# Kernel tuning notes

Measured on AMD Instinct MI355X. Metric: run time of the kernel, lower is better.

The kernel has to match this reference:

```python
import jax, jax.numpy as jnp
import numpy as np

LN_EPS = 1e-5
GATE_EPS = 1e-9
TOP_K = 2
CAP_FACTOR = 1.0


def reference(x, gamma, beta, wg, W1, b1, W2, b2):
    B, S, H = x.shape
    E = wg.shape[1]
    T = B * S
    K = TOP_K
    C = int(np.ceil(K * T / E * CAP_FACTOR))  # per-expert capacity

    xf = x.reshape(T, H)
    # LayerNorm
    mu = jnp.mean(xf, axis=-1, keepdims=True)
    var = jnp.mean(jnp.square(xf - mu), axis=-1, keepdims=True)
    xn = (xf - mu) * jax.lax.rsqrt(var + LN_EPS) * gamma + beta

    # Gating (DeepSpeed top-k gate, softmax over experts)
    logits = xn @ wg                       # [T,E]
    gates = jax.nn.softmax(logits, axis=-1)
    vals, idx = jax.lax.top_k(gates, K)    # [T,K]

    # Capacity-aware positions: slot j priorities come after slots <j counts
    counts = jnp.zeros((E,), jnp.int32)
    pos_l, keep_l = [], []
    for j in range(K):
        oh = jax.nn.one_hot(idx[:, j], E, dtype=jnp.int32)  # [T,E]
        loc = jnp.cumsum(oh, axis=0) - 1 + counts[None, :]
        pos = jnp.sum(loc * oh, axis=1)                      # [T]
        counts = counts + jnp.sum(oh, axis=0)
        pos_l.append(pos)
        keep_l.append(pos < C)
    pos_k = jnp.stack(pos_l, axis=1)                         # [T,K]
    keep_k = jnp.stack(keep_l, axis=1)                       # [T,K]

    # Normalize kept gate values (DeepSpeed normalizes after capacity drop)
    kept = vals * keep_k.astype(vals.dtype)
    w = kept / (jnp.sum(kept, axis=1, keepdims=True) + GATE_EPS)  # [T,K]

    # Load-balancing aux loss (top-1 assignment counts, DeepSpeed style)
    me = jnp.mean(gates, axis=0)
    ce = jnp.mean(jax.nn.one_hot(idx[:, 0], E, dtype=gates.dtype), axis=0)
    l_aux = jnp.mean(me * ce) * E * E

    # Dispatch: scatter tokens into [E, C+1, H]; dropped tokens go to slot C (discarded)
    buf = jnp.zeros((E, C + 1, H), xn.dtype)
    pos_pad = jnp.where(keep_k, pos_k, C)                    # [T,K]
    for j in range(K):
        buf = buf.at[idx[:, j], pos_pad[:, j]].add(xn)

    # Grouped expert MLP
    h1 = jax.nn.gelu(jnp.einsum('ech,ehf->ecf', buf, W1) + b1[:, None, :], approximate=False)
    y = jnp.einsum('ecf,efh->ech', h1, W2) + b2[:, None, :]   # [E,C+1,H]

    # Combine: gather each token's expert outputs, weight, sum
    outf = jnp.zeros((T, H), x.dtype)
    for j in range(K):
        outf = outf + w[:, j, None] * y[idx[:, j], pos_pad[:, j]]

    out = x + outf.reshape(B, S, H)
    return out, l_aux, counts.astype(jnp.float32)


def setup_inputs() -> dict:
    key = jax.random.key(0)
    ks = jax.random.split(key, 6)
    H, E, F = 1024, 8, 4096
    x = jax.random.normal(ks[0], (2, 2048, H), jnp.float32)
    return {
        'x': x,
        'gamma': jnp.ones((H,), jnp.float32),
        'beta': jnp.zeros((H,), jnp.float32),
        'wg': jax.random.normal(ks[1], (H, E), jnp.float32) * 0.02,
        'W1': jax.random.normal(ks[2], (E, H, F), jnp.float32) * 0.02,
        'b1': jnp.zeros((E, F), jnp.float32),
        'W2': jax.random.normal(ks[3], (E, F, H), jnp.float32) * 0.02,
        'b2': jnp.zeros((E, H), jnp.float32),
    }
```

## Files before the change

kernel.cpp:

```cpp
#include <hip/hip_runtime.h>
#include <hip/hip_bf16.h>
#include <math.h>


#define T_TOK 4096
#define HD 1024
#define NE 8
#define FD 4096
#define CAPN 1024

typedef __attribute__((ext_vector_type(8))) short short8;
typedef __attribute__((ext_vector_type(4))) float f32x4;

__device__ __forceinline__ unsigned short f2b(float f) {
  __hip_bfloat16 h = __float2bfloat16(f);
  unsigned short u;
  __builtin_memcpy(&u, &h, 2);
  return u;
}

__global__ __launch_bounds__(256) void k_ln_gate(
    const float* __restrict__ x, const float* __restrict__ gamma,
    const float* __restrict__ beta, const float* __restrict__ wg,
    unsigned short* __restrict__ xn, float* __restrict__ gates,
    float2* __restrict__ vals, int2* __restrict__ eidx) {
  const int t = blockIdx.x;
  const int tid = threadIdx.x;
  const int lane = tid & 63, wid = tid >> 6;
  __shared__ float red[4];
  __shared__ float pr[4][8];

  const float4 v = ((const float4*)(x + (size_t)t * HD))[tid];
  float s = v.x + v.y + v.z + v.w;
#pragma unroll
  for (int o = 32; o > 0; o >>= 1) s += __shfl_down(s, o);
  if (lane == 0) red[wid] = s;
  __syncthreads();
  const float mean = (red[0] + red[1] + red[2] + red[3]) * (1.0f / HD);
  float dv[4];
  dv[0] = v.x - mean; dv[1] = v.y - mean; dv[2] = v.z - mean; dv[3] = v.w - mean;
  float q = dv[0]*dv[0] + dv[1]*dv[1] + dv[2]*dv[2] + dv[3]*dv[3];
  __syncthreads();
#pragma unroll
  for (int o = 32; o > 0; o >>= 1) q += __shfl_down(q, o);
  if (lane == 0) red[wid] = q;
  __syncthreads();
  const float var = (red[0] + red[1] + red[2] + red[3]) * (1.0f / HD);
  const float rs = 1.0f / sqrtf(var + 1e-5f);

  const float4 gm = ((const float4*)gamma)[tid];
  const float4 bt = ((const float4*)beta)[tid];
  float xv[4];
  xv[0] = dv[0] * rs * gm.x + bt.x;
  xv[1] = dv[1] * rs * gm.y + bt.y;
  xv[2] = dv[2] * rs * gm.z + bt.z;
  xv[3] = dv[3] * rs * gm.w + bt.w;
  ushort4 o4;
  o4.x = f2b(xv[0]); o4.y = f2b(xv[1]); o4.z = f2b(xv[2]); o4.w = f2b(xv[3]);
  ((ushort4*)(xn + (size_t)t * HD))[tid] = o4;

  float p[8];
#pragma unroll
  for (int e = 0; e < 8; e++) p[e] = 0.f;
  const int c0 = tid * 4;
#pragma unroll
  for (int i = 0; i < 4; i++) {
    const float4 w0 = ((const float4*)(wg + (size_t)(c0 + i) * NE))[0];
    const float4 w1 = ((const float4*)(wg + (size_t)(c0 + i) * NE))[1];
    p[0] += xv[i] * w0.x; p[1] += xv[i] * w0.y;
    p[2] += xv[i] * w0.z; p[3] += xv[i] * w0.w;
    p[4] += xv[i] * w1.x; p[5] += xv[i] * w1.y;
    p[6] += xv[i] * w1.z; p[7] += xv[i] * w1.w;
  }
#pragma unroll
  for (int e = 0; e < 8; e++)
#pragma unroll
    for (int o = 32; o > 0; o >>= 1) p[e] += __shfl_down(p[e], o);
  if (lane == 0) {
#pragma unroll
    for (int e = 0; e < 8; e++) pr[wid][e] = p[e];
  }
  __syncthreads();
  if (tid == 0) {
    float lg[8];
#pragma unroll
    for (int e = 0; e < 8; e++) lg[e] = pr[0][e] + pr[1][e] + pr[2][e] + pr[3][e];
    float mx = lg[0];
#pragma unroll
    for (int e = 1; e < 8; e++) mx = fmaxf(mx, lg[e]);
    float ex[8], sum = 0.f;
#pragma unroll
    for (int e = 0; e < 8; e++) { ex[e] = expf(lg[e] - mx); sum += ex[e]; }
    const float inv = 1.0f / sum;
    float g[8];
#pragma unroll
    for (int e = 0; e < 8; e++) { g[e] = ex[e] * inv; gates[(size_t)t * 8 + e] = g[e]; }
    int i0 = 0;
    for (int e = 1; e < 8; e++) if (g[e] > g[i0]) i0 = e;
    int i1 = (i0 == 0) ? 1 : 0;
    for (int e = 0; e < 8; e++) if (e != i0 && g[e] > g[i1]) i1 = e;
    vals[t] = make_float2(g[i0], g[i1]);
    eidx[t] = make_int2(i0, i1);
  }
}

__global__ __launch_bounds__(256) void k_scan(
    const int2* __restrict__ eidx, const float* __restrict__ gates,
    int* __restrict__ ppad, float* __restrict__ out_tail) {
  __shared__ int s0[T_TOK], s1[T_TOK];
  __shared__ float mw[3][8];
  __shared__ int ce_sh[8], cnt_sh[8];
  const int tid = threadIdx.x;
  const int lane = tid & 63, wid = tid >> 6;
  for (int i = tid; i < T_TOK; i += 256) {
    int2 e2 = eidx[i];
    s0[i] = e2.x; s1[i] = e2.y;
  }
  __syncthreads();
  if (wid == 0) {
    const unsigned long long lt = (lane == 63) ? 0x7fffffffffffffffull
                                               : ((1ull << lane) - 1ull);
    int cnt[8];
#pragma unroll
    for (int e = 0; e < 8; e++) cnt[e] = 0;
    for (int j = 0; j < 2; j++) {
      const int* sj = j ? s1 : s0;
      for (int base = 0; base < T_TOK; base += 64) {
        const int my = sj[base + lane];
        int pos = 0;
#pragma unroll
        for (int e = 0; e < 8; e++) {
          unsigned long long m = __ballot(my == e);
          if (my == e) pos = cnt[e] + __popcll(m & lt);
          cnt[e] += __popcll(m);
        }
        ppad[(base + lane) * 2 + j] = (pos < CAPN) ? pos : CAPN;
      }
      if (j == 0 && lane == 0) {
#pragma unroll
        for (int e = 0; e < 8; e++) ce_sh[e] = cnt[e];
      }
    }
    if (lane == 0) {
#pragma unroll
      for (int e = 0; e < 8; e++) cnt_sh[e] = cnt[e];
    }
  } else {
    float acc[8];
#pragma unroll
    for (int e = 0; e < 8; e++) acc[e] = 0.f;
    for (int t = tid - 64; t < T_TOK; t += 192) {
      const float4 a = ((const float4*)(gates + (size_t)t * 8))[0];
      const float4 b = ((const float4*)(gates + (size_t)t * 8))[1];
      acc[0] += a.x; acc[1] += a.y; acc[2] += a.z; acc[3] += a.w;
      acc[4] += b.x; acc[5] += b.y; acc[6] += b.z; acc[7] += b.w;
    }
#pragma unroll
    for (int e = 0; e < 8; e++)
#pragma unroll
      for (int o = 32; o > 0; o >>= 1) acc[e] += __shfl_down(acc[e], o);
    if (lane == 0) {
#pragma unroll
      for (int e = 0; e < 8; e++) mw[wid - 1][e] = acc[e];
    }
  }
  __syncthreads();
  if (tid == 0) {
    float la = 0.f;
#pragma unroll
    for (int e = 0; e < 8; e++) {
      const float me = (mw[0][e] + mw[1][e] + mw[2][e]) * (1.0f / T_TOK);
      la += me * ((float)ce_sh[e] * (1.0f / T_TOK));
    }
    out_tail[0] = la * 8.0f;
#pragma unroll
    for (int e = 0; e < 8; e++) out_tail[1 + e] = (float)cnt_sh[e];
  }
}

__global__ __launch_bounds__(128) void k_scatter(
    const unsigned short* __restrict__ xn, const int2* __restrict__ eidx,
    const int* __restrict__ ppad, unsigned short* __restrict__ buf) {
  const int b = blockIdx.x;
  const int t = b >> 1, j = b & 1;
  const int pp = ppad[2 * t + j];
  if (pp >= CAPN) return;
  const int2 e2 = eidx[t];
  const int e = j ? e2.y : e2.x;
  const uint4* s = (const uint4*)(xn + (size_t)t * HD);
  uint4* d = (uint4*)(buf + ((size_t)e * CAPN + pp) * HD);
  d[threadIdx.x] = s[threadIdx.x];
}

__global__ __launch_bounds__(256) void k_convT(
    const float* __restrict__ Win, unsigned short* __restrict__ Wout,
    int R, int C) {
  __shared__ __align__(16) unsigned short tile[64][72];
  const int e = blockIdx.z;
  const int c0 = blockIdx.x * 64, r0 = blockIdx.y * 64;
  const int tid = threadIdx.x;
  const int r = tid >> 2, qq = tid & 3;
  const float* src = Win + ((size_t)e * R + r0 + r) * C + c0;
#pragma unroll
  for (int i = 0; i < 4; i++) {
    const int cc = qq * 16 + i * 4;
    const float4 v = *(const float4*)(src + cc);
    tile[cc + 0][r] = f2b(v.x);
    tile[cc + 1][r] = f2b(v.y);
    tile[cc + 2][r] = f2b(v.z);
    tile[cc + 3][r] = f2b(v.w);
  }
  __syncthreads();
  const int cr = tid >> 2;
  unsigned short* dst = Wout + ((size_t)e * C + c0 + cr) * R + r0 + qq * 16;
  *(uint4*)(dst + 0) = *(const uint4*)&tile[cr][qq * 16];
  *(uint4*)(dst + 8) = *(const uint4*)&tile[cr][qq * 16 + 8];
}

#define GLL16(SRC, DSTOFF) __builtin_amdgcn_global_load_lds( \
    (const __attribute__((address_space(1))) void*)(SRC), \
    (__attribute__((address_space(3))) void*)(smem + (DSTOFF)), 16, 0, 0)

#define STAGE_A(T) { const size_t ko = (size_t)(T) * 32; const int rbo = ((T)&3)*32768; \
  GLL16(gA + ko + oA0, rbo + ldsAd); \
  GLL16(gA + ko + oA1, rbo + 8192 + ldsAd); }

#define STAGE_B(T) { const size_t ko = (size_t)(T) * 32; const int rbo = ((T)&3)*32768; \
  GLL16(gB + ko + oA0, rbo + ldsBd); \
  GLL16(gB + ko + oA1, rbo + 8192 + ldsBd); }

#define TILE(T, DOST, VMW) { \
  const unsigned char* rb = smem + ((T)&3)*32768; \
  short8 af[4], bfv[4]; \
  _Pragma("unroll") for (int i = 0; i < 4; ++i) { \
    af[i]  = *(const short8*)(rb + offA + i*1024); \
    bfv[i] = *(const short8*)(rb + offB + i*1024); } \
  if (DOST) { STAGE_A((T)+3); } \
  asm volatile("s_barrier" ::: "memory"); \
  __builtin_amdgcn_s_setprio(1); \
  _Pragma("unroll") for (int mi = 0; mi < 4; ++mi) \
    _Pragma("unroll") for (int ni = 0; ni < 4; ++ni) \
      acc[mi][ni] = __builtin_amdgcn_mfma_f32_16x16x32_bf16(af[mi], bfv[ni], acc[mi][ni], 0, 0, 0); \
  __builtin_amdgcn_s_setprio(0); \
  _Pragma("unroll") for (int i = 0; i < 4; ++i) \
    af[i] = *(const short8*)(rb + offA + 4096 + i*1024); \
  if (DOST) { STAGE_B((T)+3); } \
  asm volatile("s_waitcnt lgkmcnt(0)" ::: "memory"); \
  asm volatile("s_waitcnt vmcnt(" #VMW ")" ::: "memory"); \
  asm volatile("s_barrier" ::: "memory"); \
  __builtin_amdgcn_s_setprio(1); \
  _Pragma("unroll") for (int mi = 0; mi < 4; ++mi) \
    _Pragma("unroll") for (int ni = 0; ni < 4; ++ni) \
      acc[4+mi][ni] = __builtin_amdgcn_mfma_f32_16x16x32_bf16(af[mi], bfv[ni], acc[4+mi][ni], 0, 0, 0); \
  __builtin_amdgcn_s_setprio(0); \
}

template <int MODE, int SPLITK>
__global__ __launch_bounds__(512, 2) void k_gemm256(
    const unsigned short* __restrict__ A, const unsigned short* __restrict__ Bt,
    const float* __restrict__ bias, void* __restrict__ out) {
  constexpr int K = MODE ? FD : HD;
  constexpr int N = MODE ? HD : FD;
  constexpr int KLOC = K / SPLITK;
  constexpr int NT = KLOC / 32;
  constexpr int NBT = N / 256;

  __shared__ __align__(16) unsigned char smem[4 * 32768];

  const int tid = threadIdx.x;
  const int lane = tid & 63, wid = tid >> 6;
  const int l15 = lane & 15, lq = lane >> 4;
  const int wr = wid >> 2, wc = wid & 3;

  const int nwg = gridDim.x;
  const int per = nwg >> 3;
  const int lin = blockIdx.x;
  const int swz = (lin & 7) * per + (lin >> 3);
  const int mt = swz & 31;
  const int rest = swz >> 5;
  const int nt = rest % NBT;
  const int z = rest / NBT;

  const int e = mt >> 2;
  const size_t m0 = (size_t)mt * 256;
  const int n0 = nt * 256;
  const unsigned short* gA = A + m0 * (size_t)K + (size_t)z * KLOC;
  const unsigned short* gB = Bt + ((size_t)e * N + n0) * (size_t)K + (size_t)z * KLOC;

  const int LA0 = tid * 16, LA1 = 8192 + tid * 16;
  const int r0s = LA0 >> 6, c0s = (LA0 >> 4) & 3;
  const int r1s = LA1 >> 6, c1s = (LA1 >> 4) & 3;
  const size_t oA0 = (size_t)r0s * K + (size_t)(c0s ^ ((r0s >> 1) & 3)) * 8;
  const size_t oA1 = (size_t)r1s * K + (size_t)(c1s ^ ((r1s >> 1) & 3)) * 8;
  const int ldsAd = wid * 1024;
  const int ldsBd = 16384 + wid * 1024;

  const int rA = wr * 128 + l15;
  const int offA = rA * 64 + ((lq ^ ((rA >> 1) & 3)) << 4);
  const int rB = wc * 64 + l15;
  const int offB = 16384 + rB * 64 + ((lq ^ ((rB >> 1) & 3)) << 4);

  f32x4 acc[8][4];
  const f32x4 fz = {0.f, 0.f, 0.f, 0.f};
#pragma unroll
  for (int mi = 0; mi < 8; mi++)
#pragma unroll
    for (int ni = 0; ni < 4; ni++) acc[mi][ni] = fz;

  STAGE_A(0); STAGE_B(0);
  STAGE_A(1); STAGE_B(1);
  STAGE_A(2); STAGE_B(2);
  asm volatile("s_waitcnt vmcnt(8)" ::: "memory");
  asm volatile("s_barrier" ::: "memory");

  for (int t = 0; t <= NT - 4; ++t) { TILE(t, true, 8); }
  TILE(NT - 3, false, 4);
  TILE(NT - 2, false, 0);
  TILE(NT - 1, false, 63);

  if (MODE == 0) {
    unsigned short* o = (unsigned short*)out;
    const float* brow = bias + (size_t)e * N;
#pragma unroll
    for (int mi = 0; mi < 8; ++mi)
#pragma unroll
      for (int ni = 0; ni < 4; ++ni) {
        const int col = n0 + wc * 64 + ni * 16 + l15;
        const float bv = brow[col];
#pragma unroll
        for (int r = 0; r < 4; ++r) {
          const size_t row = m0 + wr * 128 + mi * 16 + lq * 4 + r;
          const float pre = acc[mi][ni][r] + bv;
          const float g = 0.5f * pre * (1.0f + erff(pre * 0.70710678118654752f));
          o[row * (size_t)N + col] = f2b(g);
        }
      }
  } else {
    float* yp = (float*)out + (size_t)z * (8192ull * 1024ull);
#pragma unroll
    for (int mi = 0; mi < 8; ++mi)
#pragma unroll
      for (int ni = 0; ni < 4; ++ni) {
        const int col = n0 + wc * 64 + ni * 16 + l15;
#pragma unroll
        for (int r = 0; r < 4; ++r) {
          const size_t row = m0 + wr * 128 + mi * 16 + lq * 4 + r;
          yp[row * (size_t)N + col] = acc[mi][ni][r];
        }
      }
  }
}
#undef TILE
#undef STAGE_A
#undef STAGE_B
#undef GLL16

template <int SPLIT>
__global__ __launch_bounds__(256) void k_combine(
    const float* __restrict__ x, const float* __restrict__ y0,
    const float* __restrict__ y1, const float* __restrict__ b2,
    const int2* __restrict__ eidx, const int* __restrict__ ppad,
    const float2* __restrict__ vals, float* __restrict__ out) {
  const int t = blockIdx.x, tid = threadIdx.x;
  const float2 v = vals[t];
  const int2 e2 = eidx[t];
  const int p0 = ppad[2 * t], p1 = ppad[2 * t + 1];
  const float k0 = (p0 < CAPN) ? v.x : 0.f;
  const float k1 = (p1 < CAPN) ? v.y : 0.f;
  const float inv = 1.0f / (k0 + k1 + 1e-9f);
  const float w0 = k0 * inv, w1 = k1 * inv;
  float4 o = ((const float4*)(x + (size_t)t * HD))[tid];
  if (p0 < CAPN) {
    const size_t s = ((size_t)e2.x * CAPN + p0) * HD;
    float4 a = ((const float4*)(y0 + s))[tid];
    if (SPLIT == 2) {
      const float4 b = ((const float4*)(y1 + s))[tid];
      a.x += b.x; a.y += b.y; a.z += b.z; a.w += b.w;
    }
    const float4 bb = ((const float4*)(b2 + (size_t)e2.x * HD))[tid];
    o.x += w0 * (a.x + bb.x); o.y += w0 * (a.y + bb.y);
    o.z += w0 * (a.z + bb.z); o.w += w0 * (a.w + bb.w);
  }
  if (p1 < CAPN) {
    const size_t s = ((size_t)e2.y * CAPN + p1) * HD;
    float4 a = ((const float4*)(y0 + s))[tid];
    if (SPLIT == 2) {
      const float4 b = ((const float4*)(y1 + s))[tid];
      a.x += b.x; a.y += b.y; a.z += b.z; a.w += b.w;
    }
    const float4 bb = ((const float4*)(b2 + (size_t)e2.y * HD))[tid];
    o.x += w1 * (a.x + bb.x); o.y += w1 * (a.y + bb.y);
    o.z += w1 * (a.z + bb.z); o.w += w1 * (a.w + bb.w);
  }
  ((float4*)(out + (size_t)t * HD))[tid] = o;
}

extern "C" void kernel_launch(void* const* d_in, const int* in_sizes, int n_in,
                              void* d_out, int out_size, void* d_ws, size_t ws_size,
                              hipStream_t stream) {
  const float* x     = (const float*)d_in[0];
  const float* gamma = (const float*)d_in[1];
  const float* beta  = (const float*)d_in[2];
  const float* wg    = (const float*)d_in[3];
  const float* W1    = (const float*)d_in[4];
  const float* b1    = (const float*)d_in[5];
  const float* W2    = (const float*)d_in[6];
  const float* b2    = (const float*)d_in[7];
  float* out = (float*)d_out;

  char* ws = (char*)d_ws;
  float* gates        = (float*)(ws);
  float2* vals        = (float2*)(ws + (128ull << 10));
  int2* eidx          = (int2*)(ws + (160ull << 10));
  int* ppad           = (int*)(ws + (192ull << 10));
  unsigned short* xn  = (unsigned short*)(ws + (512ull << 10));
  unsigned short* buf = (unsigned short*)(ws + (512ull << 10) + (8ull << 20));
  unsigned short* h1  = (unsigned short*)(ws + (512ull << 10) + (24ull << 20));
  unsigned short* WT  = (unsigned short*)(ws + (512ull << 10) + (88ull << 20));
  float* y0           = (float*)(ws + (512ull << 10) + (152ull << 20));
  float* y1           = (float*)(ws + (512ull << 10) + (184ull << 20));
  const bool splitk = ws_size >= ((217ull << 20));

  k_ln_gate<<<T_TOK, 256, 0, stream>>>(x, gamma, beta, wg, xn, gates, vals, eidx);
  k_scan<<<1, 256, 0, stream>>>(eidx, gates, ppad, out + (size_t)T_TOK * HD);
  k_scatter<<<T_TOK * 2, 128, 0, stream>>>(xn, eidx, ppad, buf);
  k_convT<<<dim3(FD / 64, HD / 64, NE), 256, 0, stream>>>(W1, WT, HD, FD);
  k_gemm256<0, 1><<<512, 512, 0, stream>>>(buf, WT, b1, h1);
  k_convT<<<dim3(HD / 64, FD / 64, NE), 256, 0, stream>>>(W2, WT, FD, HD);
  if (splitk) {
    k_gemm256<1, 2><<<256, 512, 0, stream>>>(h1, WT, nullptr, y0);
    k_combine<2><<<T_TOK, 256, 0, stream>>>(x, y0, y1, b2, eidx, ppad, vals, out);
  } else {
    k_gemm256<1, 1><<<128, 512, 0, stream>>>(h1, WT, nullptr, y0);
    k_combine<1><<<T_TOK, 256, 0, stream>>>(x, y0, y1, b2, eidx, ppad, vals, out);
  }
}
```

Baseline: 556.4 us.

## Rewrite expert GEMM as 8-phase pipelined kernel, parallelize scan, retune transpose

The grouped expert GEMM becomes an 8-phase ping-pong schedule. It uses 64-deep K stages in two 64 KB LDS buffers with an XOR swizzle and interleaves LDS reads, global-to-LDS staging and MFMA blocks between barriers. It runs at one workgroup per CU instead of two. The single-wave capacity scan becomes a parallel chunked ballot count plus a prefix scan across 8 waves, and the convT store pattern changes to 8 threads per row. The aim is to hide memory latency behind MFMA, at the cost of lower occupancy and many more barriers.

```diff
diff --git a/kernel.cpp b/kernel.cpp
--- a/kernel.cpp
+++ b/kernel.cpp
@@ -104,77 +104,92 @@
   }
 }
 
-__global__ __launch_bounds__(256) void k_scan(
+__global__ __launch_bounds__(512) void k_scan(
     const int2* __restrict__ eidx, const float* __restrict__ gates,
     int* __restrict__ ppad, float* __restrict__ out_tail) {
-  __shared__ int s0[T_TOK], s1[T_TOK];
-  __shared__ float mw[3][8];
-  __shared__ int ce_sh[8], cnt_sh[8];
-  const int tid = threadIdx.x;
-  const int lane = tid & 63, wid = tid >> 6;
-  for (int i = tid; i < T_TOK; i += 256) {
+  __shared__ short se0[T_TOK], se1[T_TOK];
+  __shared__ int cc[2][64][8];
+  __shared__ int cb[2][64][8];
+  __shared__ float gsum[8][8];
+  __shared__ int ctot[8], c0tot[8];
+  const int tid = threadIdx.x, lane = tid & 63, wid = tid >> 6;
+  for (int i = tid; i < T_TOK; i += 512) {
     int2 e2 = eidx[i];
-    s0[i] = e2.x; s1[i] = e2.y;
-  }
-  __syncthreads();
-  if (wid == 0) {
+    se0[i] = (short)e2.x; se1[i] = (short)e2.y;
+  }
+  __syncthreads();
+  for (int c = wid * 8; c < wid * 8 + 8; ++c) {
+    const int t = c * 64 + lane;
+    const int e0 = se0[t], e1 = se1[t];
+#pragma unroll
+    for (int e = 0; e < 8; ++e) {
+      unsigned long long m0 = __ballot(e0 == e);
+      unsigned long long m1 = __ballot(e1 == e);
+      if (lane == e) { cc[0][c][e] = __popcll(m0); cc[1][c][e] = __popcll(m1); }
+    }
+  }
+  __syncthreads();
+  {
+    const int e = wid;
+    int v0 = cc[0][lane][e], v1 = cc[1][lane][e];
+    int p0 = v0, p1 = v1;
+#pragma unroll
+    for (int o = 1; o < 64; o <<= 1) {
+      int u0 = __shfl_up(p0, o), u1 = __shfl_up(p1, o);
+      if (lane >= o) { p0 += u0; p1 += u1; }
+    }
+    const int tot0 = __shfl(p0, 63), tot1 = __shfl(p1, 63);
+    cb[0][lane][e] = p0 - v0;
+    cb[1][lane][e] = p1 - v1 + tot0;
+    if (lane == 0) { c0tot[e] = tot0; ctot[e] = tot0 + tot1; }
+  }
+  __syncthreads();
+  for (int c = wid * 8; c < wid * 8 + 8; ++c) {
+    const int t = c * 64 + lane;
     const unsigned long long lt = (lane == 63) ? 0x7fffffffffffffffull
                                                : ((1ull << lane) - 1ull);
-    int cnt[8];
-#pragma unroll
-    for (int e = 0; e < 8; e++) cnt[e] = 0;
-    for (int j = 0; j < 2; j++) {
-      const int* sj = j ? s1 : s0;
-      for (int base = 0; base < T_TOK; base += 64) {
-        const int my = sj[base + lane];
-        int pos = 0;
-#pragma unroll
-        for (int e = 0; e < 8; e++) {
-          unsigned long long m = __ballot(my == e);
-          if (my == e) pos = cnt[e] + __popcll(m & lt);
-          cnt[e] += __popcll(m);
-        }
-        ppad[(base + lane) * 2 + j] = (pos < CAPN) ? pos : CAPN;
-      }
-      if (j == 0 && lane == 0) {
-#pragma unroll
-        for (int e = 0; e < 8; e++) ce_sh[e] = cnt[e];
-      }
-    }
-    if (lane == 0) {
-#pragma unroll
-      for (int e = 0; e < 8; e++) cnt_sh[e] = cnt[e];
-    }
-  } else {
-    float acc[8];
-#pragma unroll
-    for (int e = 0; e < 8; e++) acc[e] = 0.f;
-    for (int t = tid - 64; t < T_TOK; t += 192) {
-      const float4 a = ((const float4*)(gates + (size_t)t * 8))[0];
-      const float4 b = ((const float4*)(gates + (size_t)t * 8))[1];
-      acc[0] += a.x; acc[1] += a.y; acc[2] += a.z; acc[3] += a.w;
-      acc[4] += b.x; acc[5] += b.y; acc[6] += b.z; acc[7] += b.w;
-    }
-#pragma unroll
-    for (int e = 0; e < 8; e++)
-#pragma unroll
-      for (int o = 32; o > 0; o >>= 1) acc[e] += __shfl_down(acc[e], o);
-    if (lane == 0) {
-#pragma unroll
-      for (int e = 0; e < 8; e++) mw[wid - 1][e] = acc[e];
-    }
+    const int e0 = se0[t], e1 = se1[t];
+    int p0 = 0, p1 = 0;
+#pragma unroll
+    for (int e = 0; e < 8; ++e) {
+      unsigned long long m0 = __ballot(e0 == e);
+      unsigned long long m1 = __ballot(e1 == e);
+      if (e0 == e) p0 = cb[0][c][e] + __popcll(m0 & lt);
+      if (e1 == e) p1 = cb[1][c][e] + __popcll(m1 & lt);
+    }
+    ppad[2 * t]     = (p0 < CAPN) ? p0 : CAPN;
+    ppad[2 * t + 1] = (p1 < CAPN) ? p1 : CAPN;
+  }
+  float acc[8];
+#pragma unroll
+  for (int e = 0; e < 8; ++e) acc[e] = 0.f;
+  for (int t = tid; t < T_TOK; t += 512) {
+    const float4 a = ((const float4*)(gates + (size_t)t * 8))[0];
+    const float4 b = ((const float4*)(gates + (size_t)t * 8))[1];
+    acc[0] += a.x; acc[1] += a.y; acc[2] += a.z; acc[3] += a.w;
+    acc[4] += b.x; acc[5] += b.y; acc[6] += b.z; acc[7] += b.w;
+  }
+#pragma unroll
+  for (int e = 0; e < 8; ++e)
+#pragma unroll
+    for (int o = 32; o > 0; o >>= 1) acc[e] += __shfl_down(acc[e], o);
+  if (lane == 0) {
+#pragma unroll
+    for (int e = 0; e < 8; ++e) gsum[wid][e] = acc[e];
   }
   __syncthreads();
   if (tid == 0) {
     float la = 0.f;
 #pragma unroll
-    for (int e = 0; e < 8; e++) {
-      const float me = (mw[0][e] + mw[1][e] + mw[2][e]) * (1.0f / T_TOK);
-      la += me * ((float)ce_sh[e] * (1.0f / T_TOK));
+    for (int e = 0; e < 8; ++e) {
+      float sg = 0.f;
+#pragma unroll
+      for (int w = 0; w < 8; ++w) sg += gsum[w][e];
+      la += (sg * (1.0f / T_TOK)) * ((float)c0tot[e] * (1.0f / T_TOK));
     }
     out_tail[0] = la * 8.0f;
 #pragma unroll
-    for (int e = 0; e < 8; e++) out_tail[1 + e] = (float)cnt_sh[e];
+    for (int e = 0; e < 8; ++e) out_tail[1 + e] = (float)ctot[e];
   }
 }
 
@@ -211,65 +226,74 @@
     tile[cc + 3][r] = f2b(v.w);
   }
   __syncthreads();
-  const int cr = tid >> 2;
-  unsigned short* dst = Wout + ((size_t)e * C + c0 + cr) * R + r0 + qq * 16;
-  *(uint4*)(dst + 0) = *(const uint4*)&tile[cr][qq * 16];
-  *(uint4*)(dst + 8) = *(const uint4*)&tile[cr][qq * 16 + 8];
-}
-
-#define GLL16(SRC, DSTOFF) __builtin_amdgcn_global_load_lds( \
-    (const __attribute__((address_space(1))) void*)(SRC), \
-    (__attribute__((address_space(3))) void*)(smem + (DSTOFF)), 16, 0, 0)
-
-#define STAGE_A(T) { const size_t ko = (size_t)(T) * 32; const int rbo = ((T)&3)*32768; \
-  GLL16(gA + ko + oA0, rbo + ldsAd); \
-  GLL16(gA + ko + oA1, rbo + 8192 + ldsAd); }
-
-#define STAGE_B(T) { const size_t ko = (size_t)(T) * 32; const int rbo = ((T)&3)*32768; \
-  GLL16(gB + ko + oA0, rbo + ldsBd); \
-  GLL16(gB + ko + oA1, rbo + 8192 + ldsBd); }
-
-#define TILE(T, DOST, VMW) { \
-  const unsigned char* rb = smem + ((T)&3)*32768; \
-  short8 af[4], bfv[4]; \
-  _Pragma("unroll") for (int i = 0; i < 4; ++i) { \
-    af[i]  = *(const short8*)(rb + offA + i*1024); \
-    bfv[i] = *(const short8*)(rb + offB + i*1024); } \
-  if (DOST) { STAGE_A((T)+3); } \
-  asm volatile("s_barrier" ::: "memory"); \
-  __builtin_amdgcn_s_setprio(1); \
-  _Pragma("unroll") for (int mi = 0; mi < 4; ++mi) \
-    _Pragma("unroll") for (int ni = 0; ni < 4; ++ni) \
-      acc[mi][ni] = __builtin_amdgcn_mfma_f32_16x16x32_bf16(af[mi], bfv[ni], acc[mi][ni], 0, 0, 0); \
-  __builtin_amdgcn_s_setprio(0); \
-  _Pragma("unroll") for (int i = 0; i < 4; ++i) \
-    af[i] = *(const short8*)(rb + offA + 4096 + i*1024); \
-  if (DOST) { STAGE_B((T)+3); } \
-  asm volatile("s_waitcnt lgkmcnt(0)" ::: "memory"); \
-  asm volatile("s_waitcnt vmcnt(" #VMW ")" ::: "memory"); \
-  asm volatile("s_barrier" ::: "memory"); \
-  __builtin_amdgcn_s_setprio(1); \
-  _Pragma("unroll") for (int mi = 0; mi < 4; ++mi) \
-    _Pragma("unroll") for (int ni = 0; ni < 4; ++ni) \
-      acc[4+mi][ni] = __builtin_amdgcn_mfma_f32_16x16x32_bf16(af[mi], bfv[ni], acc[4+mi][ni], 0, 0, 0); \
-  __builtin_amdgcn_s_setprio(0); \
-}
+  const int cr = tid >> 3, q8 = tid & 7;
+  unsigned short* dst0 = Wout + ((size_t)e * C + c0 + cr) * R + r0 + q8 * 8;
+  *(uint4*)dst0 = *(const uint4*)&tile[cr][q8 * 8];
+  unsigned short* dst1 = Wout + ((size_t)e * C + c0 + cr + 32) * R + r0 + q8 * 8;
+  *(uint4*)dst1 = *(const uint4*)&tile[cr + 32][q8 * 8];
+}
+
+#define GLL(SRCP, DOFF) __builtin_amdgcn_global_load_lds( \
+    (const __attribute__((address_space(1))) void*)(SRCP), \
+    (__attribute__((address_space(3))) void*)(smem + (DOFF)), 16, 0, 0)
+
+#define ST_A(S, KO) { \
+  GLL(gA + (size_t)(KO) + stOff,             (S)*65536 + wid*1024); \
+  GLL(gA + (size_t)(KO) + stOff + 64*LDK,    (S)*65536 + 8192 + wid*1024); \
+  GLL(gA + (size_t)(KO) + stOff + 128*LDK,   (S)*65536 + 16384 + wid*1024); \
+  GLL(gA + (size_t)(KO) + stOff + 192*LDK,   (S)*65536 + 24576 + wid*1024); }
+
+#define ST_B(S, KO) { \
+  GLL(gB + (size_t)(KO) + stOff,             (S)*65536 + 32768 + wid*1024); \
+  GLL(gB + (size_t)(KO) + stOff + 64*LDK,    (S)*65536 + 40960 + wid*1024); \
+  GLL(gB + (size_t)(KO) + stOff + 128*LDK,   (S)*65536 + 49152 + wid*1024); \
+  GLL(gB + (size_t)(KO) + stOff + 192*LDK,   (S)*65536 + 57344 + wid*1024); }
+
+#define RD_A(S, MH) { _Pragma("unroll") for (int f = 0; f < 4; ++f) { \
+    aR[f*2+0] = *(const short8*)(smem + (S)*65536 + wrBase + ((MH)*4+f)*2048 + loff0); \
+    aR[f*2+1] = *(const short8*)(smem + (S)*65536 + wrBase + ((MH)*4+f)*2048 + loff1); } }
+
+#define RD_B(S, NH) { _Pragma("unroll") for (int g = 0; g < 2; ++g) { \
+    bR[NH][g*2+0] = *(const short8*)(smem + (S)*65536 + 32768 + bBase + ((NH)*2+g)*2048 + loff0); \
+    bR[NH][g*2+1] = *(const short8*)(smem + (S)*65536 + 32768 + bBase + ((NH)*2+g)*2048 + loff1); } }
+
+#define MM(MH, NH) { __builtin_amdgcn_s_setprio(1); \
+  _Pragma("unroll") for (int f = 0; f < 4; ++f) \
+  _Pragma("unroll") for (int g = 0; g < 2; ++g) { \
+    acc[(MH)*4+f][(NH)*2+g] = __builtin_amdgcn_mfma_f32_16x16x32_bf16(aR[f*2+0], bR[NH][g*2+0], acc[(MH)*4+f][(NH)*2+g], 0, 0, 0); \
+    acc[(MH)*4+f][(NH)*2+g] = __builtin_amdgcn_mfma_f32_16x16x32_bf16(aR[f*2+1], bR[NH][g*2+1], acc[(MH)*4+f][(NH)*2+g], 0, 0, 0); } \
+  __builtin_amdgcn_s_setprio(0); }
+
+#define BARR __builtin_amdgcn_s_barrier()
+#define LG0 asm volatile("s_waitcnt lgkmcnt(0)" ::: "memory")
+#define VM8 asm volatile("s_waitcnt vmcnt(8)" ::: "memory")
+#define VM0 asm volatile("s_waitcnt vmcnt(0)" ::: "memory")
+
+#define ITER8(DOST, VM4TXT, VM8TXT, KK2, KK3) { \
+  RD_A(0, 0); RD_B(0, 0); BARR; LG0; MM(0, 0); BARR; \
+  RD_B(0, 1);             BARR; LG0; MM(0, 1); BARR; \
+  RD_A(0, 1); if (DOST) { ST_B(0, KK2); } BARR; LG0; MM(1, 1); BARR; \
+  if (DOST) { ST_A(0, KK2); } BARR; MM(1, 0); VM4TXT; BARR; \
+  RD_A(1, 0); RD_B(1, 0); BARR; LG0; MM(0, 0); BARR; \
+  RD_B(1, 1);             BARR; LG0; MM(0, 1); BARR; \
+  RD_A(1, 1); if (DOST) { ST_B(1, KK3); } BARR; LG0; MM(1, 1); BARR; \
+  if (DOST) { ST_A(1, KK3); } BARR; MM(1, 0); VM8TXT; BARR; }
 
 template <int MODE, int SPLITK>
-__global__ __launch_bounds__(512, 2) void k_gemm256(
+__global__ __launch_bounds__(512, 1) void k_gemm8p(
     const unsigned short* __restrict__ A, const unsigned short* __restrict__ Bt,
     const float* __restrict__ bias, void* __restrict__ out) {
-  constexpr int K = MODE ? FD : HD;
+  constexpr int LDK = MODE ? FD : HD;
   constexpr int N = MODE ? HD : FD;
-  constexpr int KLOC = K / SPLITK;
-  constexpr int NT = KLOC / 32;
+  constexpr int KLOC = LDK / SPLITK;
+  constexpr int NI = KLOC / 128;
   constexpr int NBT = N / 256;
 
-  __shared__ __align__(16) unsigned char smem[4 * 32768];
+  __shared__ __align__(16) unsigned char smem[131072];
 
   const int tid = threadIdx.x;
   const int lane = tid & 63, wid = tid >> 6;
-  const int l15 = lane & 15, lq = lane >> 4;
+  const int l15 = lane & 15, lq = (lane >> 4) & 3;
   const int wr = wid >> 2, wc = wid & 3;
 
   const int nwg = gridDim.x;
@@ -284,22 +308,18 @@
   const int e = mt >> 2;
   const size_t m0 = (size_t)mt * 256;
   const int n0 = nt * 256;
-  const unsigned short* gA = A + m0 * (size_t)K + (size_t)z * KLOC;
-  const unsigned short* gB = Bt + ((size_t)e * N + n0) * (size_t)K + (size_t)z * KLOC;
-
-  const int LA0 = tid * 16, LA1 = 8192 + tid * 16;
-  const int r0s = LA0 >> 6, c0s = (LA0 >> 4) & 3;
-  const int r1s = LA1 >> 6, c1s = (LA1 >> 4) & 3;
-  const size_t oA0 = (size_t)r0s * K + (size_t)(c0s ^ ((r0s >> 1) & 3)) * 8;
-  const size_t oA1 = (size_t)r1s * K + (size_t)(c1s ^ ((r1s >> 1) & 3)) * 8;
-  const int ldsAd = wid * 1024;
-  const int ldsBd = 16384 + wid * 1024;
-
-  const int rA = wr * 128 + l15;
-  const int offA = rA * 64 + ((lq ^ ((rA >> 1) & 3)) << 4);
-  const int rB = wc * 64 + l15;
-  const int offB = 16384 + rB * 64 + ((lq ^ ((rB >> 1) & 3)) << 4);
-
+  const unsigned short* gA = A + m0 * (size_t)LDK + (size_t)z * KLOC;
+  const unsigned short* gB = Bt + ((size_t)e * N + n0) * (size_t)LDK + (size_t)z * KLOC;
+
+  const int stOff = (tid >> 3) * LDK + (((tid & 7) ^ ((tid >> 3) & 7)) << 3);
+
+  const int loff0 = l15 * 128 + (((0 + lq) ^ (l15 & 7)) << 4);
+  const int loff1 = l15 * 128 + (((4 + lq) ^ (l15 & 7)) << 4);
+  const int wrBase = wr * 16384;
+  const int bBase = (wc >> 1) * 16384 + (wc & 1) * 8192;
+
+  short8 aR[8];
+  short8 bR[2][8];
   f32x4 acc[8][4];
   const f32x4 fz = {0.f, 0.f, 0.f, 0.f};
 #pragma unroll
@@ -307,17 +327,18 @@
 #pragma unroll
     for (int ni = 0; ni < 4; ni++) acc[mi][ni] = fz;
 
-  STAGE_A(0); STAGE_B(0);
-  STAGE_A(1); STAGE_B(1);
-  STAGE_A(2); STAGE_B(2);
-  asm volatile("s_waitcnt vmcnt(8)" ::: "memory");
-  asm volatile("s_barrier" ::: "memory");
-
-  for (int t = 0; t <= NT - 4; ++t) { TILE(t, true, 8); }
-  TILE(NT - 3, false, 4);
-  TILE(NT - 2, false, 0);
-  TILE(NT - 1, false, 63);
-
+  ST_A(0, 0); ST_B(0, 0);
+  ST_A(1, 64); ST_B(1, 64);
+  VM8; BARR;
+
+  int kk = 0;
+  for (int it = 0; it < NI - 1; ++it, kk += 128) {
+    ITER8(true, VM8, VM8, kk + 128, kk + 192);
+  }
+  ITER8(false, VM0, , 0, 0);
+
+  const int colB = n0 + wc * 64 + l15;
+  const size_t rowB = m0 + (size_t)wr * 128 + lq * 4;
   if (MODE == 0) {
     unsigned short* o = (unsigned short*)out;
     const float* brow = bias + (size_t)e * N;
@@ -325,11 +346,11 @@
     for (int mi = 0; mi < 8; ++mi)
 #pragma unroll
       for (int ni = 0; ni < 4; ++ni) {
-        const int col = n0 + wc * 64 + ni * 16 + l15;
+        const int col = colB + ni * 16;
         const float bv = brow[col];
 #pragma unroll
         for (int r = 0; r < 4; ++r) {
-          const size_t row = m0 + wr * 128 + mi * 16 + lq * 4 + r;
+          const size_t row = rowB + mi * 16 + r;
           const float pre = acc[mi][ni][r] + bv;
           const float g = 0.5f * pre * (1.0f + erff(pre * 0.70710678118654752f));
           o[row * (size_t)N + col] = f2b(g);
@@ -341,19 +362,26 @@
     for (int mi = 0; mi < 8; ++mi)
 #pragma unroll
       for (int ni = 0; ni < 4; ++ni) {
-        const int col = n0 + wc * 64 + ni * 16 + l15;
+        const int col = colB + ni * 16;
 #pragma unroll
         for (int r = 0; r < 4; ++r) {
-          const size_t row = m0 + wr * 128 + mi * 16 + lq * 4 + r;
+          const size_t row = rowB + mi * 16 + r;
           yp[row * (size_t)N + col] = acc[mi][ni][r];
         }
       }
   }
 }
-#undef TILE
-#undef STAGE_A
-#undef STAGE_B
-#undef GLL16
+#undef ITER8
+#undef VM0
+#undef VM8
+#undef LG0
+#undef BARR
+#undef MM
+#undef RD_B
+#undef RD_A
+#undef ST_B
+#undef ST_A
+#undef GLL
 
 template <int SPLIT>
 __global__ __launch_bounds__(256) void k_combine(
@@ -422,16 +450,16 @@
   const bool splitk = ws_size >= ((217ull << 20));
 
   k_ln_gate<<<T_TOK, 256, 0, stream>>>(x, gamma, beta, wg, xn, gates, vals, eidx);
-  k_scan<<<1, 256, 0, stream>>>(eidx, gates, ppad, out + (size_t)T_TOK * HD);
+  k_scan<<<1, 512, 0, stream>>>(eidx, gates, ppad, out + (size_t)T_TOK * HD);
   k_scatter<<<T_TOK * 2, 128, 0, stream>>>(xn, eidx, ppad, buf);
   k_convT<<<dim3(FD / 64, HD / 64, NE), 256, 0, stream>>>(W1, WT, HD, FD);
-  k_gemm256<0, 1><<<512, 512, 0, stream>>>(buf, WT, b1, h1);
+  k_gemm8p<0, 1><<<512, 512, 0, stream>>>(buf, WT, b1, h1);
   k_convT<<<dim3(HD / 64, FD / 64, NE), 256, 0, stream>>>(W2, WT, FD, HD);
   if (splitk) {
-    k_gemm256<1, 2><<<256, 512, 0, stream>>>(h1, WT, nullptr, y0);
+    k_gemm8p<1, 2><<<256, 512, 0, stream>>>(h1, WT, nullptr, y0);
     k_combine<2><<<T_TOK, 256, 0, stream>>>(x, y0, y1, b2, eidx, ppad, vals, out);
   } else {
-    k_gemm256<1, 1><<<128, 512, 0, stream>>>(h1, WT, nullptr, y0);
+    k_gemm8p<1, 1><<<128, 512, 0, stream>>>(h1, WT, nullptr, y0);
     k_combine<1><<<T_TOK, 256, 0, stream>>>(x, y0, y1, b2, eidx, ppad, vals, out);
   }
 }
```

After: 530.9 us. 4.6% less time.
